# Kernel optimization log

Hardware: AMD Instinct MI355X
Metric: run time of the kernel (lower is better)

The kernel has to match this reference:

```python
import jax, jax.numpy as jnp
import numpy as np

NUM_NODES = 100000
NUM_EDGES = 2500000
NUM_GRAPHS = 512
NODE_DIM = 7
STATE_DIM = 32
M = 2
ROUNDS = 4


def setup_inputs() -> dict:
    key = jax.random.key(0)
    ks = jax.random.split(key, 16)
    x = jax.random.normal(ks[0], (NUM_NODES, NODE_DIM), dtype=jnp.float32)
    edge_index = jax.random.randint(ks[1], (2, NUM_EDGES), 0, NUM_NODES)
    batch = jnp.sort(jax.random.randint(ks[2], (NUM_NODES,), 0, NUM_GRAPHS))
    s = 1.0 / np.sqrt(STATE_DIM)
    W_in = jax.random.normal(ks[3], (NODE_DIM, STATE_DIM), dtype=jnp.float32) / np.sqrt(NODE_DIM)
    b_in = jnp.zeros((STATE_DIM,), dtype=jnp.float32)
    W_msg = jax.random.normal(ks[4], (ROUNDS, STATE_DIM, STATE_DIM), dtype=jnp.float32) * s
    b_msg = jnp.zeros((ROUNDS, STATE_DIM), dtype=jnp.float32)
    W_upd = jax.random.normal(ks[5], (ROUNDS, STATE_DIM, STATE_DIM), dtype=jnp.float32) * s
    b_upd = jnp.zeros((ROUNDS, STATE_DIM), dtype=jnp.float32)
    W_out = jax.random.normal(ks[6], (STATE_DIM, 2 * M), dtype=jnp.float32) * s
    b_out = jnp.zeros((2 * M,), dtype=jnp.float32)
    return {"x": x, "edge_index": edge_index, "batch": batch,
            "W_in": W_in, "b_in": b_in, "W_msg": W_msg, "b_msg": b_msg,
            "W_upd": W_upd, "b_upd": b_upd, "W_out": W_out, "b_out": b_out}


def reference(x, edge_index, batch, W_in, b_in, W_msg, b_msg, W_upd, b_upd, W_out, b_out):
    # input net
    state = jax.nn.relu(x @ W_in + b_in)  # (N, S)
    src, dst = edge_index[0], edge_index[1]
    for r in range(ROUNDS):
        message = jax.nn.relu(state @ W_msg[r] + b_msg[r])          # (N, S)
        gathered = message[src]                                      # (E, S) irregular gather
        aggregated = jax.ops.segment_sum(gathered, dst, num_segments=NUM_NODES)  # scatter-add
        state = state + jax.nn.relu(aggregated @ W_upd[r] + b_upd[r])
    graph_state = jax.ops.segment_sum(state, batch, num_segments=NUM_GRAPHS)     # (G, S)
    out = graph_state @ W_out + b_out                                # (G, 2M)
    mean, log_std = jnp.split(out, 2, axis=-1)
    # Gaussian head: return mean and std (scale = exp(log_std)) concatenated
    return jnp.concatenate([mean, jnp.exp(log_std)], axis=-1)
```

## Files before the change

kernel.cpp:

```cpp
#include <hip/hip_runtime.h>
#include <hip/hip_fp8.h>
#include <math.h>

#define N_NODES 100000
#define N_EDGES 2500000
#define N_GRAPHS 512
#define NODE_DIM 7
#define S 32
#define ROUNDS 4

#define BKT_SHIFT 7
#define BKT_NODES 128
#define NBKT ((N_NODES + BKT_NODES - 1) / BKT_NODES)
#define CAP 3712
#define NSLOT 64
#define SLOT_PAD 32

#define GN (N_NODES * S / 256)
#define GG (N_NODES / 16)

__device__ __forceinline__ void block_max_publish(float v, float* slots, int bid, int tid) {
    __shared__ float wmax[4];
#pragma unroll
    for (int o = 32; o > 0; o >>= 1) v = fmaxf(v, __shfl_xor(v, o, 64));
    if ((tid & 63) == 0) wmax[tid >> 6] = v;
    __syncthreads();
    if (tid == 0) {
        float m = fmaxf(fmaxf(wmax[0], wmax[1]), fmaxf(wmax[2], wmax[3]));
        atomicMax((unsigned int*)&slots[(bid & (NSLOT - 1)) * SLOT_PAD], __float_as_uint(m));
    }
}

__device__ __forceinline__ void acc4_fp8(unsigned int u, float& a0, float& a1,
                                         float& a2, float& a3) {
#if __has_builtin(__builtin_amdgcn_cvt_pk_f32_fp8)
    typedef float v2f __attribute__((ext_vector_type(2)));
    v2f lo = __builtin_amdgcn_cvt_pk_f32_fp8((int)u, false);
    v2f hi = __builtin_amdgcn_cvt_pk_f32_fp8((int)u, true);
    a0 += lo.x; a1 += lo.y; a2 += hi.x; a3 += hi.y;
#else
    __hip_fp8_e4m3 t0, t1, t2, t3;
    t0.__x = u & 0xff; t1.__x = (u >> 8) & 0xff;
    t2.__x = (u >> 16) & 0xff; t3.__x = (u >> 24) & 0xff;
    a0 += (float)t0; a1 += (float)t1; a2 += (float)t2; a3 += (float)t3;
#endif
}

__global__ void k_input(const float* __restrict__ x, const float* __restrict__ W_in,
                        const float* __restrict__ b_in, float* __restrict__ state,
                        float* __restrict__ graph_state, int* __restrict__ cursor,
                        float* __restrict__ smax0) {
    __shared__ float sW[NODE_DIM * S];
    __shared__ float sb[S];
    int tid = threadIdx.x;
    if (tid < NODE_DIM * S) sW[tid] = W_in[tid];
    if (tid < S) sb[tid] = b_in[tid];
    __syncthreads();
    int gid = blockIdx.x * blockDim.x + tid;
    if (gid < N_GRAPHS * S) graph_state[gid] = 0.f;
    if (gid < NBKT) cursor[gid] = 0;
    int n = gid >> 5, j = gid & 31;
    float acc = sb[j];
#pragma unroll
    for (int k = 0; k < NODE_DIM; k++) acc += x[n * NODE_DIM + k] * sW[k * S + j];
    float v = fmaxf(acc, 0.f);
    state[gid] = v;
    block_max_publish(v, smax0, blockIdx.x, tid);
}

__global__ void k_bin(const int* __restrict__ src, const int* __restrict__ dst,
                      int* __restrict__ cursor, int* __restrict__ binned) {
    __shared__ int cnt[NBKT];
    __shared__ int base[NBKT];
    int tile = (N_EDGES + gridDim.x - 1) / gridDim.x;
    int b0 = blockIdx.x * tile;
    int b1 = min(b0 + tile, N_EDGES);
    for (int i = threadIdx.x; i < NBKT; i += blockDim.x) cnt[i] = 0;
    __syncthreads();
    for (int e = b0 + threadIdx.x; e < b1; e += blockDim.x)
        atomicAdd(&cnt[dst[e] >> BKT_SHIFT], 1);
    __syncthreads();
    for (int i = threadIdx.x; i < NBKT; i += blockDim.x) {
        int c = cnt[i];
        base[i] = c ? atomicAdd(&cursor[i], c) : 0;
        cnt[i] = 0;
    }
    __syncthreads();
    for (int e = b0 + threadIdx.x; e < b1; e += blockDim.x) {
        int d = dst[e];
        int k = d >> BKT_SHIFT;
        int lpos = base[k] + atomicAdd(&cnt[k], 1);
        if (lpos < CAP)
            binned[(size_t)k * CAP + lpos] = (src[e] << BKT_SHIFT) | (d & (BKT_NODES - 1));
    }
}

__global__ void k_fill2(const int* __restrict__ cursor, int* __restrict__ binned,
                        int* __restrict__ row_beg, int* __restrict__ row_end) {
    __shared__ int stage[CAP];
    __shared__ int cnt[BKT_NODES];
    __shared__ int sm[BKT_NODES];
    int tid = threadIdx.x;
    int bkt = blockIdx.x;
    int beg = bkt * CAP;
    int m = min(cursor[bkt], CAP);
    for (int i = tid; i < m; i += 256) stage[i] = binned[beg + i];
    if (tid < BKT_NODES) cnt[tid] = 0;
    __syncthreads();
    for (int i = tid; i < m; i += 256) atomicAdd(&cnt[stage[i] & (BKT_NODES - 1)], 1);
    __syncthreads();
    int v = 0;
    if (tid < BKT_NODES) { v = cnt[tid]; sm[tid] = v; }
    __syncthreads();
    for (int off = 1; off < BKT_NODES; off <<= 1) {
        int add = 0;
        if (tid < BKT_NODES && tid >= off) add = sm[tid - off];
        __syncthreads();
        if (tid < BKT_NODES) sm[tid] += add;
        __syncthreads();
    }
    if (tid < BKT_NODES) {
        int excl = sm[tid] - v;
        cnt[tid] = excl;
        int n = bkt * BKT_NODES + tid;
        if (n < N_NODES) { row_beg[n] = beg + excl; row_end[n] = beg + excl + v; }
    }
    __syncthreads();
    for (int i = tid; i < m; i += 256) {
        int ent = stage[i];
        int p = atomicAdd(&cnt[ent & (BKT_NODES - 1)], 1);
        binned[beg + p] = ent >> BKT_SHIFT;
    }
}

__global__ void k_msg(const float* __restrict__ state, const float* __restrict__ W,
                      const float* __restrict__ b, const float* __restrict__ smax_slots,
                      float* __restrict__ inv_scale_out,
                      __hip_fp8_e4m3* __restrict__ message) {
    __shared__ float sW[S * S];
    __shared__ float sb[S];
    __shared__ float ssc[S];
    int tid = threadIdx.x;
    for (int i = tid; i < S * S; i += 256) sW[i] = W[i];
    if (tid < S) sb[tid] = b[tid];
    __syncthreads();
    if (tid < S) {
        float smax = 0.f;
#pragma unroll
        for (int k = 0; k < NSLOT; k++) smax = fmaxf(smax, smax_slots[k * SLOT_PAD]);
        float cs = 0.f;
#pragma unroll
        for (int k = 0; k < S; k++) cs += fabsf(sW[k * S + tid]);
        float bound = smax * cs + fabsf(sb[tid]) + 1e-20f;
        int e = (int)floorf(log2f(400.f / bound));
        e = max(-60, min(60, e));
        ssc[tid] = exp2f((float)e);
        if (blockIdx.x == 0) inv_scale_out[tid] = exp2f((float)-e);
    }
    __syncthreads();
    int gid = blockIdx.x * 256 + tid;
    int j = tid & 31;
    float my = state[gid];
    float acc = sb[j];
#pragma unroll
    for (int k = 0; k < S; k++) acc += __shfl(my, k, 32) * sW[k * S + j];
    float m = fminf(fmaxf(acc, 0.f) * ssc[j], 440.f);
    message[gid] = __hip_fp8_e4m3(m);
}

__global__ void k_gather_upd(const int* __restrict__ row_beg, const int* __restrict__ row_end,
                             const int* __restrict__ csr_src,
                             const unsigned char* __restrict__ message,
                             const float* __restrict__ W, const float* __restrict__ b,
                             const float* __restrict__ inv_scale,
                             float* __restrict__ state, float* __restrict__ smax_next) {
    __shared__ float sW[S * S];
    __shared__ float sb[S];
    __shared__ float si[S];
    int tid = threadIdx.x;
    for (int i = tid; i < S * S; i += 256) sW[i] = W[i];
    if (tid < S) { sb[tid] = b[tid]; si[tid] = inv_scale[tid]; }
    __syncthreads();
    int g = tid >> 5, j = tid & 31;
    int n0 = blockIdx.x * 16 + g * 2;
    int n1 = n0 + 1;
    int es = j >> 3;
    int qd = j & 7;
    int b0 = row_beg[n0], e0 = row_end[n0];
    int b1 = row_beg[n1], e1 = row_end[n1];
    float a0 = 0.f, a1 = 0.f, a2 = 0.f, a3 = 0.f;
    float c0 = 0.f, c1 = 0.f, c2 = 0.f, c3 = 0.f;
    for (; b0 < e0 || b1 < e1; b0 += 32, b1 += 32) {
        int sid0 = (b0 + j < e0) ? csr_src[b0 + j] : 0;
        int sid1 = (b1 + j < e1) ? csr_src[b1 + j] : 0;
        unsigned int u0[8], u1[8];
#pragma unroll
        for (int p = 0; p < 8; p++) {
            int s = __shfl(sid0, p * 4 + es, 32);
            unsigned int* ap = (unsigned int*)(message + (unsigned)s * 32u + (unsigned)qd * 4u);
            u0[p] = __hip_atomic_load(ap, __ATOMIC_RELAXED, __HIP_MEMORY_SCOPE_AGENT);
        }
#pragma unroll
        for (int p = 0; p < 8; p++) {
            int s = __shfl(sid1, p * 4 + es, 32);
            unsigned int* ap = (unsigned int*)(message + (unsigned)s * 32u + (unsigned)qd * 4u);
            u1[p] = __hip_atomic_load(ap, __ATOMIC_RELAXED, __HIP_MEMORY_SCOPE_AGENT);
        }
#pragma unroll
        for (int p = 0; p < 8; p++) {
            unsigned int uv = (b0 + p * 4 + es < e0) ? u0[p] : 0u;
            acc4_fp8(uv, a0, a1, a2, a3);
        }
#pragma unroll
        for (int p = 0; p < 8; p++) {
            unsigned int uv = (b1 + p * 4 + es < e1) ? u1[p] : 0u;
            acc4_fp8(uv, c0, c1, c2, c3);
        }
    }
    a0 += __shfl_xor(a0, 8, 32); a0 += __shfl_xor(a0, 16, 32);
    a1 += __shfl_xor(a1, 8, 32); a1 += __shfl_xor(a1, 16, 32);
    a2 += __shfl_xor(a2, 8, 32); a2 += __shfl_xor(a2, 16, 32);
    a3 += __shfl_xor(a3, 8, 32); a3 += __shfl_xor(a3, 16, 32);
    c0 += __shfl_xor(c0, 8, 32); c0 += __shfl_xor(c0, 16, 32);
    c1 += __shfl_xor(c1, 8, 32); c1 += __shfl_xor(c1, 16, 32);
    c2 += __shfl_xor(c2, 8, 32); c2 += __shfl_xor(c2, 16, 32);
    c3 += __shfl_xor(c3, 8, 32); c3 += __shfl_xor(c3, 16, 32);
    float s0 = si[4 * qd + 0], s1 = si[4 * qd + 1];
    float s2 = si[4 * qd + 2], s3 = si[4 * qd + 3];
    a0 *= s0; a1 *= s1; a2 *= s2; a3 *= s3;
    c0 *= s0; c1 *= s1; c2 *= s2; c3 *= s3;
    float u0v = sb[j], u1v = sb[j];
#pragma unroll
    for (int k = 0; k < S; k++) {
        float av, cv;
        switch (k & 3) {
            case 0: av = __shfl(a0, k >> 2, 32); cv = __shfl(c0, k >> 2, 32); break;
            case 1: av = __shfl(a1, k >> 2, 32); cv = __shfl(c1, k >> 2, 32); break;
            case 2: av = __shfl(a2, k >> 2, 32); cv = __shfl(c2, k >> 2, 32); break;
            default: av = __shfl(a3, k >> 2, 32); cv = __shfl(c3, k >> 2, 32); break;
        }
        float w = sW[k * S + j];
        u0v += av * w;
        u1v += cv * w;
    }
    size_t i0 = (size_t)n0 * S + j, i1 = (size_t)n1 * S + j;
    float ns0 = state[i0] + fmaxf(u0v, 0.f);
    float ns1 = state[i1] + fmaxf(u1v, 0.f);
    state[i0] = ns0;
    state[i1] = ns1;
    block_max_publish(fmaxf(ns0, ns1), smax_next, blockIdx.x, tid);
}

__global__ void k_pool(const float* __restrict__ state, const int* __restrict__ batch,
                       float* __restrict__ graph_state) {
    const int CHUNK = 32;
    const int nchunks = (N_NODES + CHUNK - 1) / CHUNK;
    int gid = blockIdx.x * blockDim.x + threadIdx.x;
    if (gid >= nchunks * S) return;
    int c = gid >> 5, j = gid & 31;
    int n0 = c * CHUNK;
    int n1 = min(n0 + CHUNK, N_NODES);
    float acc = 0.f;
    int curb = batch[n0];
    for (int n = n0; n < n1; n++) {
        int bn = batch[n];
        if (bn != curb) {
            atomicAdd(&graph_state[curb * S + j], acc);
            acc = 0.f;
            curb = bn;
        }
        acc += state[(size_t)n * S + j];
    }
    atomicAdd(&graph_state[curb * S + j], acc);
}

__global__ void k_head(const float* __restrict__ graph_state, const float* __restrict__ W_out,
                       const float* __restrict__ b_out, float* __restrict__ out) {
    int gid = blockIdx.x * blockDim.x + threadIdx.x;
    if (gid >= N_GRAPHS * 4) return;
    int g = gid >> 2, j = gid & 3;
    float acc = b_out[j];
#pragma unroll
    for (int k = 0; k < S; k++) acc += graph_state[g * S + k] * W_out[k * 4 + j];
    out[gid] = (j < 2) ? acc : expf(fminf(acc, 88.0f));
}

extern "C" void kernel_launch(void* const* d_in, const int* in_sizes, int n_in,
                              void* d_out, int out_size, void* d_ws, size_t ws_size,
                              hipStream_t stream) {
    const float* x     = (const float*)d_in[0];
    const int*   ei    = (const int*)d_in[1];
    const int*   batch = (const int*)d_in[2];
    const float* W_in  = (const float*)d_in[3];
    const float* b_in  = (const float*)d_in[4];
    const float* W_msg = (const float*)d_in[5];
    const float* b_msg = (const float*)d_in[6];
    const float* W_upd = (const float*)d_in[7];
    const float* b_upd = (const float*)d_in[8];
    const float* W_out = (const float*)d_in[9];
    const float* b_out = (const float*)d_in[10];
    float* out = (float*)d_out;

    float* state            = (float*)d_ws;
    __hip_fp8_e4m3* message = (__hip_fp8_e4m3*)(state + (size_t)N_NODES * S);
    float* graph_state      = (float*)((char*)message + (size_t)N_NODES * S);
    float* smax             = graph_state + N_GRAPHS * S;
    float* inv_scale        = smax + (ROUNDS + 1) * NSLOT * SLOT_PAD;
    int*   row_beg          = (int*)(inv_scale + S);
    int*   row_end          = row_beg + N_NODES;
    int*   cursor           = row_end + N_NODES;
    int*   binned           = cursor + NBKT;

    const int* src = ei;
    const int* dst = ei + N_EDGES;

    hipMemsetAsync(smax, 0, (ROUNDS + 1) * NSLOT * SLOT_PAD * sizeof(float), stream);
    k_input<<<GN, dim3(256), 0, stream>>>(x, W_in, b_in, state, graph_state, cursor, smax);
    k_bin<<<256, dim3(1024), 0, stream>>>(src, dst, cursor, binned);
    k_fill2<<<NBKT, dim3(256), 0, stream>>>(cursor, binned, row_beg, row_end);

    for (int r = 0; r < ROUNDS; r++) {
        k_msg<<<GN, dim3(256), 0, stream>>>(state, W_msg + r * S * S, b_msg + r * S,
                                            smax + r * NSLOT * SLOT_PAD, inv_scale, message);
        k_gather_upd<<<GG, dim3(256), 0, stream>>>(row_beg, row_end, binned,
                                                   (const unsigned char*)message,
                                                   W_upd + r * S * S, b_upd + r * S,
                                                   inv_scale, state,
                                                   smax + (r + 1) * NSLOT * SLOT_PAD);
    }

    const int CHUNK = 32;
    int nchunks = (N_NODES + CHUNK - 1) / CHUNK;
    int gP = (nchunks * S + 255) / 256;
    k_pool<<<gP, dim3(256), 0, stream>>>(state, batch, graph_state);

    k_head<<<(N_GRAPHS * 4 + 255) / 256, dim3(256), 0, stream>>>(graph_state, W_out, b_out, out);
}
```

Measured before the change: 369.9 us.

## Drop smax memset, register-cache dst in binning, prefetch next CSR indices

Removes the hipMemsetAsync of the smax slots. k_input now writes per-block maxima to a temp buffer, k_bin block 0 reduces them into slot 0 and clears the other slots, and each k_msg clears the next round's slots. k_bin keeps its ten dst values per thread in registers so dst is read once instead of twice. k_gather_upd prefetches the next 32 source indices while the current fp8 gathers are in flight. The gains are one fewer launch and less latency, but correctness now depends on ordering: k_msg must clear the next slots before the following gather kernel publishes to them.

```diff
diff --git a/kernel.cpp b/kernel.cpp
--- a/kernel.cpp
+++ b/kernel.cpp
@@ -49,9 +49,10 @@
 __global__ void k_input(const float* __restrict__ x, const float* __restrict__ W_in,
                         const float* __restrict__ b_in, float* __restrict__ state,
                         float* __restrict__ graph_state, int* __restrict__ cursor,
-                        float* __restrict__ smax0) {
+                        float* __restrict__ tmpmax) {
     __shared__ float sW[NODE_DIM * S];
     __shared__ float sb[S];
+    __shared__ float wmax[4];
     int tid = threadIdx.x;
     if (tid < NODE_DIM * S) sW[tid] = W_in[tid];
     if (tid < S) sb[tid] = b_in[tid];
@@ -65,33 +66,66 @@
     for (int k = 0; k < NODE_DIM; k++) acc += x[n * NODE_DIM + k] * sW[k * S + j];
     float v = fmaxf(acc, 0.f);
     state[gid] = v;
-    block_max_publish(v, smax0, blockIdx.x, tid);
+#pragma unroll
+    for (int o = 32; o > 0; o >>= 1) v = fmaxf(v, __shfl_xor(v, o, 64));
+    if ((tid & 63) == 0) wmax[tid >> 6] = v;
+    __syncthreads();
+    if (tid == 0)
+        tmpmax[blockIdx.x] = fmaxf(fmaxf(wmax[0], wmax[1]), fmaxf(wmax[2], wmax[3]));
 }
 
 __global__ void k_bin(const int* __restrict__ src, const int* __restrict__ dst,
-                      int* __restrict__ cursor, int* __restrict__ binned) {
+                      int* __restrict__ cursor, int* __restrict__ binned,
+                      const float* __restrict__ tmpmax, float* __restrict__ smax0) {
     __shared__ int cnt[NBKT];
     __shared__ int base[NBKT];
+    __shared__ float red[16];
+    int tid = threadIdx.x;
+    if (blockIdx.x == 0) {
+        float m = 0.f;
+        for (int i = tid; i < GN; i += 1024) m = fmaxf(m, tmpmax[i]);
+#pragma unroll
+        for (int o = 32; o > 0; o >>= 1) m = fmaxf(m, __shfl_xor(m, o, 64));
+        if ((tid & 63) == 0) red[tid >> 6] = m;
+        __syncthreads();
+        if (tid == 0) {
+            float g = 0.f;
+#pragma unroll
+            for (int k = 0; k < 16; k++) g = fmaxf(g, red[k]);
+            smax0[0] = g;
+        } else if (tid < NSLOT) {
+            smax0[tid * SLOT_PAD] = 0.f;
+        }
+    }
     int tile = (N_EDGES + gridDim.x - 1) / gridDim.x;
     int b0 = blockIdx.x * tile;
     int b1 = min(b0 + tile, N_EDGES);
-    for (int i = threadIdx.x; i < NBKT; i += blockDim.x) cnt[i] = 0;
-    __syncthreads();
-    for (int e = b0 + threadIdx.x; e < b1; e += blockDim.x)
-        atomicAdd(&cnt[dst[e] >> BKT_SHIFT], 1);
-    __syncthreads();
-    for (int i = threadIdx.x; i < NBKT; i += blockDim.x) {
+    for (int i = tid; i < NBKT; i += blockDim.x) cnt[i] = 0;
+    __syncthreads();
+    int dv[10];
+#pragma unroll
+    for (int q = 0; q < 10; q++) {
+        int e = b0 + tid + q * 1024;
+        dv[q] = (e < b1) ? dst[e] : -1;
+        if (dv[q] >= 0) atomicAdd(&cnt[dv[q] >> BKT_SHIFT], 1);
+    }
+    __syncthreads();
+    for (int i = tid; i < NBKT; i += blockDim.x) {
         int c = cnt[i];
         base[i] = c ? atomicAdd(&cursor[i], c) : 0;
         cnt[i] = 0;
     }
     __syncthreads();
-    for (int e = b0 + threadIdx.x; e < b1; e += blockDim.x) {
-        int d = dst[e];
-        int k = d >> BKT_SHIFT;
-        int lpos = base[k] + atomicAdd(&cnt[k], 1);
-        if (lpos < CAP)
-            binned[(size_t)k * CAP + lpos] = (src[e] << BKT_SHIFT) | (d & (BKT_NODES - 1));
+#pragma unroll
+    for (int q = 0; q < 10; q++) {
+        int e = b0 + tid + q * 1024;
+        int d = dv[q];
+        if (d >= 0) {
+            int k = d >> BKT_SHIFT;
+            int lpos = base[k] + atomicAdd(&cnt[k], 1);
+            if (lpos < CAP)
+                binned[(size_t)k * CAP + lpos] = (src[e] << BKT_SHIFT) | (d & (BKT_NODES - 1));
+        }
     }
 }
 
@@ -135,12 +169,13 @@
 
 __global__ void k_msg(const float* __restrict__ state, const float* __restrict__ W,
                       const float* __restrict__ b, const float* __restrict__ smax_slots,
-                      float* __restrict__ inv_scale_out,
+                      float* __restrict__ smax_next, float* __restrict__ inv_scale_out,
                       __hip_fp8_e4m3* __restrict__ message) {
     __shared__ float sW[S * S];
     __shared__ float sb[S];
     __shared__ float ssc[S];
     int tid = threadIdx.x;
+    if (blockIdx.x < NSLOT && tid == 0) smax_next[blockIdx.x * SLOT_PAD] = 0.f;
     for (int i = tid; i < S * S; i += 256) sW[i] = W[i];
     if (tid < S) sb[tid] = b[tid];
     __syncthreads();
@@ -190,9 +225,9 @@
     int b1 = row_beg[n1], e1 = row_end[n1];
     float a0 = 0.f, a1 = 0.f, a2 = 0.f, a3 = 0.f;
     float c0 = 0.f, c1 = 0.f, c2 = 0.f, c3 = 0.f;
-    for (; b0 < e0 || b1 < e1; b0 += 32, b1 += 32) {
-        int sid0 = (b0 + j < e0) ? csr_src[b0 + j] : 0;
-        int sid1 = (b1 + j < e1) ? csr_src[b1 + j] : 0;
+    int sid0 = (b0 + j < e0) ? csr_src[b0 + j] : 0;
+    int sid1 = (b1 + j < e1) ? csr_src[b1 + j] : 0;
+    while (b0 < e0 || b1 < e1) {
         unsigned int u0[8], u1[8];
 #pragma unroll
         for (int p = 0; p < 8; p++) {
@@ -206,6 +241,9 @@
             unsigned int* ap = (unsigned int*)(message + (unsigned)s * 32u + (unsigned)qd * 4u);
             u1[p] = __hip_atomic_load(ap, __ATOMIC_RELAXED, __HIP_MEMORY_SCOPE_AGENT);
         }
+        int nb0 = b0 + 32, nb1 = b1 + 32;
+        int nsid0 = (nb0 + j < e0) ? csr_src[nb0 + j] : 0;
+        int nsid1 = (nb1 + j < e1) ? csr_src[nb1 + j] : 0;
 #pragma unroll
         for (int p = 0; p < 8; p++) {
             unsigned int uv = (b0 + p * 4 + es < e0) ? u0[p] : 0u;
@@ -216,6 +254,7 @@
             unsigned int uv = (b1 + p * 4 + es < e1) ? u1[p] : 0u;
             acc4_fp8(uv, c0, c1, c2, c3);
         }
+        b0 = nb0; b1 = nb1; sid0 = nsid0; sid1 = nsid1;
     }
     a0 += __shfl_xor(a0, 8, 32); a0 += __shfl_xor(a0, 16, 32);
     a1 += __shfl_xor(a1, 8, 32); a1 += __shfl_xor(a1, 16, 32);
@@ -306,7 +345,8 @@
     float* graph_state      = (float*)((char*)message + (size_t)N_NODES * S);
     float* smax             = graph_state + N_GRAPHS * S;
     float* inv_scale        = smax + (ROUNDS + 1) * NSLOT * SLOT_PAD;
-    int*   row_beg          = (int*)(inv_scale + S);
+    float* tmpmax           = inv_scale + S;
+    int*   row_beg          = (int*)(tmpmax + GN);
     int*   row_end          = row_beg + N_NODES;
     int*   cursor           = row_end + N_NODES;
     int*   binned           = cursor + NBKT;
@@ -314,14 +354,15 @@
     const int* src = ei;
     const int* dst = ei + N_EDGES;
 
-    hipMemsetAsync(smax, 0, (ROUNDS + 1) * NSLOT * SLOT_PAD * sizeof(float), stream);
-    k_input<<<GN, dim3(256), 0, stream>>>(x, W_in, b_in, state, graph_state, cursor, smax);
-    k_bin<<<256, dim3(1024), 0, stream>>>(src, dst, cursor, binned);
+    k_input<<<GN, dim3(256), 0, stream>>>(x, W_in, b_in, state, graph_state, cursor, tmpmax);
+    k_bin<<<256, dim3(1024), 0, stream>>>(src, dst, cursor, binned, tmpmax, smax);
     k_fill2<<<NBKT, dim3(256), 0, stream>>>(cursor, binned, row_beg, row_end);
 
     for (int r = 0; r < ROUNDS; r++) {
         k_msg<<<GN, dim3(256), 0, stream>>>(state, W_msg + r * S * S, b_msg + r * S,
-                                            smax + r * NSLOT * SLOT_PAD, inv_scale, message);
+                                            smax + r * NSLOT * SLOT_PAD,
+                                            smax + (r + 1) * NSLOT * SLOT_PAD,
+                                            inv_scale, message);
         k_gather_upd<<<GG, dim3(256), 0, stream>>>(row_beg, row_end, binned,
                                                    (const unsigned char*)message,
                                                    W_upd + r * S * S, b_upd + r * S,
```

Result: no change. 369.9 us (-0.0%).
